# Kernel tuning notes

Hardware: AMD Instinct MI355X
Metric: run time of the kernel (lower is better)

The kernel has to match this reference:

```python
import jax, jax.numpy as jnp
import numpy as np

# Dimensions
B = 2          # batch
WIN = 8
S = WIN * WIN  # 64 tokens in the window
C = 64         # embed_dim (per-head channel dim)
NH = 8         # num_heads
H, W = 32, 32  # per-token spatial field
M1, M2 = 16, 16  # retained Fourier modes


def _spectral_conv(x, w):
    """FNO-style spectral conv over the last two dims.
    x: [B, S, Cin, H, W] real; w: [Cin, Cout, M1, M2, 2] (real/imag parts).
    rfft2 -> truncate to (M1, M2) modes -> complex channel mixing -> irfft2.
    """
    wc = w[..., 0] + 1j * w[..., 1]                      # [Cin, Cout, M1, M2]
    xf = jnp.fft.rfft2(x)                                # [B, S, Cin, H, W//2+1]
    of = jnp.einsum('bsixy,ioxy->bsoxy', xf[..., :M1, :M2], wc)
    out_f = jnp.zeros(xf.shape[:2] + (wc.shape[1], H, W // 2 + 1), dtype=of.dtype)
    out_f = out_f.at[..., :M1, :M2].set(of)
    return jnp.fft.irfft2(out_f, s=(H, W))               # [B, S, Cout, H, W]


def _log_cpb(w1, b1, w2, b2):
    """Swin-v2 style log-spaced continuous position bias.
    MLP(2 -> C -> NH) on log-spaced relative coords of the WIN x WIN window.
    Returns [NH, S, S].
    """
    g = jnp.arange(WIN)
    coords = jnp.stack(jnp.meshgrid(g, g, indexing='ij'), 0).reshape(2, -1)   # [2, S]
    rel = (coords[:, :, None] - coords[:, None, :]).astype(jnp.float32)       # [2, S, S]
    rel = jnp.transpose(rel, (1, 2, 0)) * (8.0 / (WIN - 1))                   # [S, S, 2]
    rel = jnp.sign(rel) * jnp.log2(jnp.abs(rel) + 1.0) / np.float32(np.log2(8.0))
    h = jax.nn.relu(rel @ w1 + b1)                                            # [S, S, C]
    bias = h @ w2 + b2                                                        # [S, S, NH]
    return 16.0 * jax.nn.sigmoid(jnp.transpose(bias, (2, 0, 1)))              # [NH, S, S]


def setup_inputs() -> dict:
    key = jax.random.key(0)
    k = jax.random.split(key, 8)
    def rn(kk, shape, s):
        return jax.random.normal(kk, shape, jnp.float32) * np.float32(s)
    return {
        'seq': jax.random.normal(k[0], (B, S, C, H, W), jnp.float32),
        'wq': rn(k[1], (C, C * NH, M1, M2, 2), 1.0 / C),
        'wk': rn(k[2], (C, C * NH, M1, M2, 2), 1.0 / C),
        'wv': rn(k[3], (C, C * NH, M1, M2, 2), 1.0 / C),
        'wo': rn(k[4], (C * NH, C, M1, M2, 2), 1.0 / (C * NH)),
        'cpb_w1': rn(k[5], (2, C), 0.1),
        'cpb_b1': jnp.zeros((C,), jnp.float32),
        'cpb_w2': rn(k[6], (C, NH), 0.1),
        'cpb_b2': jnp.zeros((NH,), jnp.float32),
    }


def reference(seq, wq, wk, wv, wo, cpb_w1, cpb_b1, cpb_w2, cpb_b2):
    # Spectral QKV projections: C -> NH*C channels
    q = _spectral_conv(seq, wq)   # [B, S, NH*C, H, W]
    kk = _spectral_conv(seq, wk)
    v = _spectral_conv(seq, wv)

    def unfl(f):  # [B, S, NH*C, H, W] -> [B, NH, S, C, H, W]
        return jnp.transpose(f.reshape(B, S, NH, C, H, W), (0, 2, 1, 3, 4, 5))

    q, kk, v = unfl(q), unfl(kk), unfl(v)

    bias = _log_cpb(cpb_w1, cpb_b1, cpb_w2, cpb_b2)      # [NH, S, S]
    scale = np.float32(1.0 / np.sqrt(C * H * W))
    scores = jnp.einsum('bhsdxy,bhtdxy->bhst', q, kk) * scale + bias
    attn = jax.nn.softmax(scores, axis=-1)               # [B, NH, S, S]
    o = jnp.einsum('bhst,bhtdxy->bhsdxy', attn, v)       # [B, NH, S, C, H, W]

    o = jnp.transpose(o, (0, 2, 1, 3, 4, 5)).reshape(B, S, NH * C, H, W)
    return _spectral_conv(o, wo)                         # [B, S, C, H, W]
```

## Files before the change

kernel.cpp:

```cpp
#include <hip/hip_runtime.h>
#include <math.h>


#define PI_F 3.14159265358979323846f

typedef _Float16 f16;
typedef f16 f16x8 __attribute__((ext_vector_type(8)));
typedef f16 f16x4 __attribute__((ext_vector_type(4)));
typedef float f32x4 __attribute__((ext_vector_type(4)));

#define MFMA(a, b, c) __builtin_amdgcn_mfma_f32_16x16x32_f16(a, b, c, 0, 0, 0)

__device__ __forceinline__ int swz128(int row, int slot) {
  return (row << 7) + (((slot) ^ (row & 7)) << 4);
}
__device__ __forceinline__ int swzel(int row, int col) {
  return (row << 7) + ((((col) >> 3) ^ (row & 7)) << 4) + (((col) & 7) << 1);
}

__global__ __launch_bounds__(256) void k_dft(const float* __restrict__ seq,
                                             f16* __restrict__ Xr,
                                             f16* __restrict__ Xi) {
  __shared__ float fld[32][33];
  __shared__ float2 tb[32][17];
  __shared__ float2 tw[32];
  int f = blockIdx.x;
  int tid = threadIdx.x;
  if (tid < 32) {
    float a = (2.0f * PI_F / 32.0f) * (float)tid;
    tw[tid] = make_float2(cosf(a), sinf(a));
  }
  const float4* s4 = (const float4*)(seq + (size_t)f * 1024);
  float4 v = s4[tid];
  int x0 = tid >> 3, y0 = (tid & 7) * 4;
  fld[x0][y0 + 0] = v.x; fld[x0][y0 + 1] = v.y;
  fld[x0][y0 + 2] = v.z; fld[x0][y0 + 3] = v.w;
  __syncthreads();
  for (int o = tid; o < 512; o += 256) {
    int x = o >> 4, q = o & 15;
    float re = 0.f, im = 0.f;
#pragma unroll
    for (int y = 0; y < 32; ++y) {
      float val = fld[x][y];
      float2 w = tw[(q * y) & 31];
      re = fmaf(val, w.x, re);
      im = fmaf(val, -w.y, im);
    }
    tb[x][q] = make_float2(re, im);
  }
  __syncthreads();
  int p = tid >> 4, q = tid & 15;
  float re = 0.f, im = 0.f;
#pragma unroll
  for (int x = 0; x < 32; ++x) {
    float2 t = tb[x][q];
    float2 w = tw[(p * x) & 31];
    re += w.x * t.x + w.y * t.y;
    im += w.x * t.y - w.y * t.x;
  }
  int b = f >> 12;
  int si = f & 4095;
  size_t o = (size_t)(b * 256 + tid) * 4096 + si;
  Xr[o] = (f16)re;
  Xi[o] = (f16)im;
}

__global__ __launch_bounds__(256) void k_repack_all(
    const float2* __restrict__ wq, const float2* __restrict__ wk,
    const float2* __restrict__ wv, const float2* __restrict__ wo,
    f16* __restrict__ Pqr, f16* __restrict__ Pqi, f16* __restrict__ Pkr,
    f16* __restrict__ Pki, f16* __restrict__ Pvr, f16* __restrict__ Pvi,
    f16* __restrict__ Por, f16* __restrict__ Poi) {
  __shared__ f16 tR[32][264];
  __shared__ f16 tI[32][264];
  int gid = blockIdx.x;
  int tsel = gid >> 10, rblk = gid & 1023;
  int m0 = (rblk & 7) << 5;
  int pc = rblk >> 3;
  const float2* in;
  f16 *oR, *oI;
  if (tsel == 0) { in = wq; oR = Pqr; oI = Pqi; }
  else if (tsel == 1) { in = wk; oR = Pkr; oI = Pki; }
  else if (tsel == 2) { in = wv; oR = Pvr; oI = Pvi; }
  else { in = wo; oR = Por; oI = Poi; }
  int tid = threadIdx.x;
  const float4* in4 = (const float4*)in;
#pragma unroll
  for (int it = 0; it < 16; ++it) {
    int k = it * 256 + tid;
    int fq = k & 15, rr = k >> 4;
    int row;
    if (tsel == 3) row = (((pc & 1) * 256 + rr) * 64) + (pc >> 1);
    else row = (rr & 63) * 512 + pc * 4 + (rr >> 6);
    float4 v = in4[(size_t)row * 128 + (m0 >> 1) + fq];
    int sw = (fq & 7) << 3;
    tR[2 * fq + 0][rr ^ sw] = (f16)v.x;
    tI[2 * fq + 0][rr ^ sw] = (f16)v.y;
    tR[2 * fq + 1][rr ^ sw] = (f16)v.z;
    tI[2 * fq + 1][rr ^ sw] = (f16)v.w;
  }
  __syncthreads();
  bool scaled = (tsel == 0) || (tsel == 2);
#pragma unroll
  for (int it = 0; it < 8; ++it) {
    int s = it * 256 + tid;
    int pl = s >> 10, mi = (s >> 5) & 31, j = s & 31;
    int sw = ((mi >> 1) & 7) << 3;
    f16x8 v = pl ? *(const f16x8*)&tI[mi][(j * 8) ^ sw]
                 : *(const f16x8*)&tR[mi][(j * 8) ^ sw];
    int mode = m0 + mi;
    if (scaled) {
      f16 scl = (mode == 0) ? (f16)1.0f
                            : (((mode & 15) == 0) ? (f16)0.5f : (f16)2.0f);
      v = v * scl;
      if (pl && mode == 0) v = (f16x8)(f16)0.0f;
    }
    f16* dst = pl ? oI : oR;
    *(f16x8*)&dst[(size_t)mode * 32768 + pc * 256 + j * 8] = v;
  }
}

__global__ __launch_bounds__(256, 2) void k_scores_m(
    const f16* __restrict__ Xr, const f16* __restrict__ Xi,
    const f16* __restrict__ Qwr, const f16* __restrict__ Qwi,
    const f16* __restrict__ Kwr, const f16* __restrict__ Kwi,
    float* __restrict__ scores) {
  __shared__ __align__(16) unsigned char smem[65536];
  const int P_WQR = 0, P_WQI = 8192, P_WKR = 16384, P_WKI = 24576;
  const int P_QR = 32768, P_QI = 40960, P_KR = 49152, P_KI = 57344;
  int tid = threadIdx.x;
  int w = tid >> 6, lane = tid & 63, r = lane & 15, g = lane >> 4;
  int wr = w >> 1, wc = w & 1;
  int chunk = blockIdx.x, h = blockIdx.y;
  f32x4 S[2][2][2] = {};
  for (int mm = 0; mm < 4; ++mm) {
    int m = chunk * 4 + mm;
    const float4* gqr = (const float4*)Qwr + (size_t)m * 4096 + h * 512;
    const float4* gqi = (const float4*)Qwi + (size_t)m * 4096 + h * 512;
    const float4* gkr = (const float4*)Kwr + (size_t)m * 4096 + h * 512;
    const float4* gki = (const float4*)Kwi + (size_t)m * 4096 + h * 512;
#pragma unroll
    for (int it = 0; it < 2; ++it) {
      int s = tid + it * 256;
      int lo = swz128(s >> 3, s & 7);
      *(float4*)(smem + P_WQR + lo) = gqr[s];
      *(float4*)(smem + P_WQI + lo) = gqi[s];
      *(float4*)(smem + P_WKR + lo) = gkr[s];
      *(float4*)(smem + P_WKI + lo) = gki[s];
    }
    __syncthreads();
#pragma unroll
    for (int b = 0; b < 2; ++b) {
      const f16x8* xr8 = (const f16x8*)Xr + (size_t)(b * 256 + m) * 512;
      const f16x8* xi8 = (const f16x8*)Xi + (size_t)(b * 256 + m) * 512;
      f16x8 axr[2][2], axi[2][2];
#pragma unroll
      for (int rt = 0; rt < 2; ++rt)
#pragma unroll
        for (int kt = 0; kt < 2; ++kt) {
          int idx = (32 * wr + rt * 16 + r) * 8 + kt * 4 + g;
          axr[rt][kt] = xr8[idx];
          axi[rt][kt] = xi8[idx];
        }
      {
        f32x4 cr[2][2] = {}, ci[2][2] = {};
#pragma unroll
        for (int ct = 0; ct < 2; ++ct)
#pragma unroll
          for (int kt = 0; kt < 2; ++kt) {
            int lo = swz128(32 * wc + ct * 16 + r, kt * 4 + g);
            f16x8 bwr = *(const f16x8*)(smem + P_WQR + lo);
            f16x8 bwi = *(const f16x8*)(smem + P_WQI + lo);
            f16x8 bwiN = -bwi;
#pragma unroll
            for (int rt = 0; rt < 2; ++rt) {
              cr[rt][ct] = MFMA(axr[rt][kt], bwr, cr[rt][ct]);
              cr[rt][ct] = MFMA(axi[rt][kt], bwiN, cr[rt][ct]);
              ci[rt][ct] = MFMA(axr[rt][kt], bwi, ci[rt][ct]);
              ci[rt][ct] = MFMA(axi[rt][kt], bwr, ci[rt][ct]);
            }
          }
#pragma unroll
        for (int rt = 0; rt < 2; ++rt)
#pragma unroll
          for (int ct = 0; ct < 2; ++ct)
#pragma unroll
            for (int j = 0; j < 4; ++j) {
              int row = 32 * wr + rt * 16 + g * 4 + j;
              int col = 32 * wc + ct * 16 + r;
              *(f16*)(smem + P_QR + swzel(row, col)) = (f16)cr[rt][ct][j];
              *(f16*)(smem + P_QI + swzel(row, col)) = (f16)ci[rt][ct][j];
            }
      }
      {
        f32x4 cr[2][2] = {}, ci[2][2] = {};
#pragma unroll
        for (int ct = 0; ct < 2; ++ct)
#pragma unroll
          for (int kt = 0; kt < 2; ++kt) {
            int lo = swz128(32 * wc + ct * 16 + r, kt * 4 + g);
            f16x8 bwr = *(const f16x8*)(smem + P_WKR + lo);
            f16x8 bwi = *(const f16x8*)(smem + P_WKI + lo);
            f16x8 bwiN = -bwi;
#pragma unroll
            for (int rt = 0; rt < 2; ++rt) {
              cr[rt][ct] = MFMA(axr[rt][kt], bwr, cr[rt][ct]);
              cr[rt][ct] = MFMA(axi[rt][kt], bwiN, cr[rt][ct]);
              ci[rt][ct] = MFMA(axr[rt][kt], bwi, ci[rt][ct]);
              ci[rt][ct] = MFMA(axi[rt][kt], bwr, ci[rt][ct]);
            }
          }
#pragma unroll
        for (int rt = 0; rt < 2; ++rt)
#pragma unroll
          for (int ct = 0; ct < 2; ++ct)
#pragma unroll
            for (int j = 0; j < 4; ++j) {
              int row = 32 * wr + rt * 16 + g * 4 + j;
              int col = 32 * wc + ct * 16 + r;
              *(f16*)(smem + P_KR + swzel(row, col)) = (f16)cr[rt][ct][j];
              *(f16*)(smem + P_KI + swzel(row, col)) = (f16)ci[rt][ct][j];
            }
      }
      __syncthreads();
      {
        f16x8 aqr[2][2], aqi[2][2];
#pragma unroll
        for (int rt = 0; rt < 2; ++rt)
#pragma unroll
          for (int kt = 0; kt < 2; ++kt) {
            int lo = swz128(32 * wr + rt * 16 + r, kt * 4 + g);
            aqr[rt][kt] = *(const f16x8*)(smem + P_QR + lo);
            aqi[rt][kt] = *(const f16x8*)(smem + P_QI + lo);
          }
#pragma unroll
        for (int ct = 0; ct < 2; ++ct)
#pragma unroll
          for (int kt = 0; kt < 2; ++kt) {
            int lo = swz128(32 * wc + ct * 16 + r, kt * 4 + g);
            f16x8 bkr = *(const f16x8*)(smem + P_KR + lo);
            f16x8 bki = *(const f16x8*)(smem + P_KI + lo);
#pragma unroll
            for (int rt = 0; rt < 2; ++rt) {
              S[b][rt][ct] = MFMA(aqr[rt][kt], bkr, S[b][rt][ct]);
              S[b][rt][ct] = MFMA(aqi[rt][kt], bki, S[b][rt][ct]);
            }
          }
      }
      __syncthreads();
    }
  }
  const float fac = 1.0f / 262144.0f;
#pragma unroll
  for (int b = 0; b < 2; ++b) {
    float* dst = scores + ((size_t)(b * 8 + h)) * 4096;
#pragma unroll
    for (int rt = 0; rt < 2; ++rt)
#pragma unroll
      for (int ct = 0; ct < 2; ++ct)
#pragma unroll
        for (int j = 0; j < 4; ++j) {
          int s_ = 32 * wr + rt * 16 + g * 4 + j;
          int t_ = 32 * wc + ct * 16 + r;
          atomicAdd(&dst[s_ * 64 + t_], S[b][rt][ct][j] * fac);
        }
  }
}

__global__ __launch_bounds__(64) void k_softmax(const float* __restrict__ scores,
                                                const float* __restrict__ w1,
                                                const float* __restrict__ b1,
                                                const float* __restrict__ w2,
                                                const float* __restrict__ b2,
                                                f16* __restrict__ at) {
  int id = blockIdx.x;
  int s = id & 63;
  int h = (id >> 6) & 7;
  int t = threadIdx.x;
  float d0 = (float)((s >> 3) - (t >> 3)) * (8.0f / 7.0f);
  float d1 = (float)((s & 7) - (t & 7)) * (8.0f / 7.0f);
  float a0 = log2f(fabsf(d0) + 1.0f) * (1.0f / 3.0f);
  float a1 = log2f(fabsf(d1) + 1.0f) * (1.0f / 3.0f);
  float r0 = (d0 < 0.f) ? -a0 : a0;
  float r1 = (d1 < 0.f) ? -a1 : a1;
  float acc = b2[h];
  for (int c = 0; c < 64; ++c) {
    float hv = fmaf(r0, w1[c], fmaf(r1, w1[64 + c], b1[c]));
    hv = fmaxf(hv, 0.0f);
    acc = fmaf(hv, w2[c * 8 + h], acc);
  }
  float bias = 16.0f / (1.0f + expf(-acc));
  size_t base = (size_t)id * 64;
  float v = scores[base + t] + bias;
  float mx = v;
  for (int o = 32; o; o >>= 1) mx = fmaxf(mx, __shfl_xor(mx, o));
  float e = expf(v - mx);
  float sm = e;
  for (int o = 32; o; o >>= 1) sm += __shfl_xor(sm, o);
  at[base + t] = (f16)(e / sm);
}

__global__ __launch_bounds__(256, 2) void k_vpath_m(
    const f16* __restrict__ Xr, const f16* __restrict__ Xi,
    const f16* __restrict__ Vwr, const f16* __restrict__ Vwi,
    const f16* __restrict__ Owr, const f16* __restrict__ Owi,
    const f16* __restrict__ At, float2* __restrict__ Ff) {
  __shared__ __align__(16) unsigned char smem[73728];
  const int P_WVR = 0, P_WVI = 8192, P_WOR = 16384, P_WOI = 24576;
  const int P_VTR = 32768, P_VTI = 40960, P_YR = 49152, P_YI = 57344;
  const int P_AT = 65536;
  int tid = threadIdx.x;
  int w = tid >> 6, lane = tid & 63, r = lane & 15, g = lane >> 4;
  int wr = w >> 1, wc = w & 1;
  int m = blockIdx.x, b = blockIdx.y;
  const f16x8* xr8 = (const f16x8*)Xr + (size_t)(b * 256 + m) * 512;
  const f16x8* xi8 = (const f16x8*)Xi + (size_t)(b * 256 + m) * 512;
  f16x8 axr[2][2], axi[2][2], axiN[2][2];
#pragma unroll
  for (int rt = 0; rt < 2; ++rt)
#pragma unroll
    for (int kt = 0; kt < 2; ++kt) {
      int idx = (32 * wr + rt * 16 + r) * 8 + kt * 4 + g;
      axr[rt][kt] = xr8[idx];
      axi[rt][kt] = xi8[idx];
      axiN[rt][kt] = -axi[rt][kt];
    }
  f32x4 fr[2][2] = {}, fi_[2][2] = {};
  for (int h = 0; h < 8; ++h) {
    __syncthreads();
    const float4* gvr = (const float4*)Vwr + (size_t)m * 4096 + h * 512;
    const float4* gvi = (const float4*)Vwi + (size_t)m * 4096 + h * 512;
    const float4* gor = (const float4*)Owr + (size_t)m * 4096 + h * 8;
    const float4* goi = (const float4*)Owi + (size_t)m * 4096 + h * 8;
    const float4* gat = (const float4*)At + (size_t)(b * 8 + h) * 512;
#pragma unroll
    for (int it = 0; it < 2; ++it) {
      int s = tid + it * 256;
      int row = s >> 3, sl = s & 7;
      int lo = swz128(row, sl);
      *(float4*)(smem + P_WVR + lo) = gvr[s];
      *(float4*)(smem + P_WVI + lo) = gvi[s];
      *(float4*)(smem + P_WOR + lo) = gor[row * 64 + sl];
      *(float4*)(smem + P_WOI + lo) = goi[row * 64 + sl];
      *(float4*)(smem + P_AT + lo) = gat[s];
    }
    __syncthreads();
    {
      f32x4 vr[2][2] = {}, vi[2][2] = {};
#pragma unroll
      for (int ct = 0; ct < 2; ++ct)
#pragma unroll
        for (int kt = 0; kt < 2; ++kt) {
          int lo = swz128(32 * wc + ct * 16 + r, kt * 4 + g);
          f16x8 bwr = *(const f16x8*)(smem + P_WVR + lo);
          f16x8 bwi = *(const f16x8*)(smem + P_WVI + lo);
#pragma unroll
          for (int rt = 0; rt < 2; ++rt) {
            vr[rt][ct] = MFMA(axr[rt][kt], bwr, vr[rt][ct]);
            vr[rt][ct] = MFMA(axiN[rt][kt], bwi, vr[rt][ct]);
            vi[rt][ct] = MFMA(axr[rt][kt], bwi, vi[rt][ct]);
            vi[rt][ct] = MFMA(axi[rt][kt], bwr, vi[rt][ct]);
          }
        }
#pragma unroll
      for (int rt = 0; rt < 2; ++rt)
#pragma unroll
        for (int ct = 0; ct < 2; ++ct) {
          int drow = 32 * wc + ct * 16 + r;
          int t0 = 32 * wr + rt * 16 + g * 4;
          f16x4 pr, pi;
#pragma unroll
          for (int j = 0; j < 4; ++j) {
            pr[j] = (f16)vr[rt][ct][j];
            pi[j] = (f16)vi[rt][ct][j];
          }
          int lo = swzel(drow, t0);
          *(f16x4*)(smem + P_VTR + lo) = pr;
          *(f16x4*)(smem + P_VTI + lo) = pi;
        }
    }
    __syncthreads();
    {
      f16x8 aat[2][2];
#pragma unroll
      for (int rt = 0; rt < 2; ++rt)
#pragma unroll
        for (int kt = 0; kt < 2; ++kt)
          aat[rt][kt] = *(const f16x8*)(
              smem + P_AT + swz128(32 * wr + rt * 16 + r, kt * 4 + g));
      f32x4 yr[2][2] = {}, yi[2][2] = {};
#pragma unroll
      for (int ct = 0; ct < 2; ++ct)
#pragma unroll
        for (int kt = 0; kt < 2; ++kt) {
          int lo = swz128(32 * wc + ct * 16 + r, kt * 4 + g);
          f16x8 bvr = *(const f16x8*)(smem + P_VTR + lo);
          f16x8 bvi = *(const f16x8*)(smem + P_VTI + lo);
#pragma unroll
          for (int rt = 0; rt < 2; ++rt) {
            yr[rt][ct] = MFMA(aat[rt][kt], bvr, yr[rt][ct]);
            yi[rt][ct] = MFMA(aat[rt][kt], bvi, yi[rt][ct]);
          }
        }
#pragma unroll
      for (int rt = 0; rt < 2; ++rt)
#pragma unroll
        for (int ct = 0; ct < 2; ++ct)
#pragma unroll
          for (int j = 0; j < 4; ++j) {
            int row = 32 * wr + rt * 16 + g * 4 + j;
            int col = 32 * wc + ct * 16 + r;
            *(f16*)(smem + P_YR + swzel(row, col)) = (f16)yr[rt][ct][j];
            *(f16*)(smem + P_YI + swzel(row, col)) = (f16)yi[rt][ct][j];
          }
    }
    __syncthreads();
    {
      f16x8 ayr[2][2], ayi[2][2], ayiN[2][2];
#pragma unroll
      for (int rt = 0; rt < 2; ++rt)
#pragma unroll
        for (int kt = 0; kt < 2; ++kt) {
          int lo = swz128(32 * wr + rt * 16 + r, kt * 4 + g);
          ayr[rt][kt] = *(const f16x8*)(smem + P_YR + lo);
          ayi[rt][kt] = *(const f16x8*)(smem + P_YI + lo);
          ayiN[rt][kt] = -ayi[rt][kt];
        }
#pragma unroll
      for (int ct = 0; ct < 2; ++ct)
#pragma unroll
        for (int kt = 0; kt < 2; ++kt) {
          int lo = swz128(32 * wc + ct * 16 + r, kt * 4 + g);
          f16x8 bor = *(const f16x8*)(smem + P_WOR + lo);
          f16x8 boi = *(const f16x8*)(smem + P_WOI + lo);
#pragma unroll
          for (int rt = 0; rt < 2; ++rt) {
            fr[rt][ct] = MFMA(ayr[rt][kt], bor, fr[rt][ct]);
            fr[rt][ct] = MFMA(ayiN[rt][kt], boi, fr[rt][ct]);
            fi_[rt][ct] = MFMA(ayr[rt][kt], boi, fi_[rt][ct]);
            fi_[rt][ct] = MFMA(ayi[rt][kt], bor, fi_[rt][ct]);
          }
        }
    }
  }
#pragma unroll
  for (int rt = 0; rt < 2; ++rt)
#pragma unroll
    for (int ct = 0; ct < 2; ++ct)
#pragma unroll
      for (int j = 0; j < 4; ++j) {
        int s_ = 32 * wr + rt * 16 + g * 4 + j;
        int c_ = 32 * wc + ct * 16 + r;
        Ff[(((size_t)(b * 64 + s_)) * 64 + c_) * 256 + m] =
            make_float2(fr[rt][ct][j], fi_[rt][ct][j]);
      }
}

__global__ __launch_bounds__(256) void k_idft(const float2* __restrict__ Ff,
                                              float* __restrict__ out) {
  __shared__ float2 Fm[256];
  __shared__ float2 g[32][17];
  __shared__ float2 tw[32];
  int f = blockIdx.x;
  int tid = threadIdx.x;
  if (tid < 32) {
    float a = (2.0f * PI_F / 32.0f) * (float)tid;
    tw[tid] = make_float2(cosf(a), sinf(a));
  }
  Fm[tid] = Ff[(size_t)f * 256 + tid];
  __syncthreads();
  for (int o = tid; o < 512; o += 256) {
    int x = o >> 4, q = o & 15;
    float gr = 0.f, gi = 0.f;
#pragma unroll
    for (int p = 0; p < 16; ++p) {
      float2 a = Fm[p * 16 + q];
      float2 w = tw[(p * x) & 31];
      gr += a.x * w.x - a.y * w.y;
      gi += a.x * w.y + a.y * w.x;
    }
    g[x][q] = make_float2(gr, gi);
  }
  __syncthreads();
  int x = tid >> 3, j0 = (tid & 7) * 4;
  float4 r;
  float* rr = &r.x;
#pragma unroll
  for (int jj = 0; jj < 4; ++jj) {
    int j = j0 + jj;
    float acc = 0.f;
#pragma unroll
    for (int q = 0; q < 16; ++q) {
      float2 gv = g[x][q];
      float2 w = tw[(q * j) & 31];
      acc += gv.x * w.x - gv.y * w.y;
    }
    rr[jj] = acc * (1.0f / 1024.0f);
  }
  *(float4*)(out + (size_t)f * 1024 + x * 32 + j0) = r;
}

extern "C" void kernel_launch(void* const* d_in, const int* in_sizes, int n_in,
                              void* d_out, int out_size, void* d_ws,
                              size_t ws_size, hipStream_t stream) {
  const float* seq = (const float*)d_in[0];
  const float2* wq = (const float2*)d_in[1];
  const float2* wk = (const float2*)d_in[2];
  const float2* wv = (const float2*)d_in[3];
  const float2* wo = (const float2*)d_in[4];
  const float* w1 = (const float*)d_in[5];
  const float* b1 = (const float*)d_in[6];
  const float* w2 = (const float*)d_in[7];
  const float* b2 = (const float*)d_in[8];
  float* out = (float*)d_out;

  char* ws = (char*)d_ws;
  f16* Xr = (f16*)(ws + 0);
  f16* Xi = (f16*)(ws + 4194304);
  float* scores = (float*)(ws + 8388608);
  f16* At = (f16*)(ws + 8650752);
  float2* Ff = (float2*)(ws + 8781824);
  f16* Pqr = (f16*)(ws + 25559040);
  f16* Pqi = (f16*)(ws + 42336256);
  f16* Pkr = (f16*)(ws + 59113472);
  f16* Pki = (f16*)(ws + 75890688);
  f16* Pvr = (f16*)(ws + 92667904);
  f16* Pvi = (f16*)(ws + 109445120);
  f16* Por = (f16*)(ws + 126222336);
  f16* Poi = (f16*)(ws + 142999552);

  hipMemsetAsync(scores, 0, 262144, stream);
  k_dft<<<8192, 256, 0, stream>>>(seq, Xr, Xi);
  k_repack_all<<<4096, 256, 0, stream>>>(wq, wk, wv, wo, Pqr, Pqi, Pkr, Pki,
                                         Pvr, Pvi, Por, Poi);
  k_scores_m<<<dim3(64, 8), 256, 0, stream>>>(Xr, Xi, Pqr, Pqi, Pkr, Pki,
                                              scores);
  k_softmax<<<1024, 64, 0, stream>>>(scores, w1, b1, w2, b2, At);
  k_vpath_m<<<dim3(256, 2), 256, 0, stream>>>(Xr, Xi, Pvr, Pvi, Por, Poi, At,
                                              Ff);
  k_idft<<<8192, 256, 0, stream>>>(Ff, out);
}
```

Baseline: 273.4 us.

## Merge DFT/repack/scores into heterogeneous megakernels and drop shared-memory weight staging

Combines the forward DFT with the Q/K weight repack in one launch, and the V/O repack with the score computation in a second launch, so independent work can overlap inside each grid. The repack now writes a plain row-major layout, and the scores and V-path kernels read MFMA weight fragments straight from global memory instead of staging them in LDS. This cuts shared memory and removes barriers. The V-path output is written coalesced and then reordered by a new transpose kernel. The risks are uncoalesced global fragment loads, extra traffic from the transpose, and the scores blocks being scheduled after the repack blocks inside the same grid.

```diff
diff --git a/kernel.cpp b/kernel.cpp
--- a/kernel.cpp
+++ b/kernel.cpp
@@ -18,14 +18,11 @@
   return (row << 7) + ((((col) >> 3) ^ (row & 7)) << 4) + (((col) & 7) << 1);
 }
 
-__global__ __launch_bounds__(256) void k_dft(const float* __restrict__ seq,
-                                             f16* __restrict__ Xr,
-                                             f16* __restrict__ Xi) {
-  __shared__ float fld[32][33];
-  __shared__ float2 tb[32][17];
-  __shared__ float2 tw[32];
-  int f = blockIdx.x;
-  int tid = threadIdx.x;
+__device__ void dft_body(char* sm, int f, int tid, const float* __restrict__ seq,
+                         f16* __restrict__ Xr, f16* __restrict__ Xi) {
+  float(*fld)[33] = (float(*)[33])sm;
+  float2(*tb)[17] = (float2(*)[17])(sm + 4224);
+  float2* tw = (float2*)(sm + 8576);
   if (tid < 32) {
     float a = (2.0f * PI_F / 32.0f) * (float)tid;
     tw[tid] = make_float2(cosf(a), sinf(a));
@@ -65,49 +62,25 @@
   Xi[o] = (f16)im;
 }
 
-__global__ __launch_bounds__(256) void k_repack_all(
-    const float2* __restrict__ wq, const float2* __restrict__ wk,
-    const float2* __restrict__ wv, const float2* __restrict__ wo,
-    f16* __restrict__ Pqr, f16* __restrict__ Pqi, f16* __restrict__ Pkr,
-    f16* __restrict__ Pki, f16* __restrict__ Pvr, f16* __restrict__ Pvi,
-    f16* __restrict__ Por, f16* __restrict__ Poi) {
-  __shared__ f16 tR[32][264];
-  __shared__ f16 tI[32][264];
-  int gid = blockIdx.x;
-  int tsel = gid >> 10, rblk = gid & 1023;
-  int m0 = (rblk & 7) << 5;
-  int pc = rblk >> 3;
-  const float2* in;
-  f16 *oR, *oI;
-  if (tsel == 0) { in = wq; oR = Pqr; oI = Pqi; }
-  else if (tsel == 1) { in = wk; oR = Pkr; oI = Pki; }
-  else if (tsel == 2) { in = wv; oR = Pvr; oI = Pvi; }
-  else { in = wo; oR = Por; oI = Poi; }
-  int tid = threadIdx.x;
+__device__ void repack_qkv(char* sm, int tid, int r, const float2* __restrict__ in,
+                           f16* __restrict__ oR, f16* __restrict__ oI,
+                           bool scaled) {
+  f16(*tR)[72] = (f16(*)[72])sm;
+  f16(*tI)[72] = (f16(*)[72])(sm + 9216);
+  int m0 = (r & 3) * 64, bb = r >> 2;
   const float4* in4 = (const float4*)in;
-#pragma unroll
-  for (int it = 0; it < 16; ++it) {
-    int k = it * 256 + tid;
-    int fq = k & 15, rr = k >> 4;
-    int row;
-    if (tsel == 3) row = (((pc & 1) * 256 + rr) * 64) + (pc >> 1);
-    else row = (rr & 63) * 512 + pc * 4 + (rr >> 6);
-    float4 v = in4[(size_t)row * 128 + (m0 >> 1) + fq];
-    int sw = (fq & 7) << 3;
-    tR[2 * fq + 0][rr ^ sw] = (f16)v.x;
-    tI[2 * fq + 0][rr ^ sw] = (f16)v.y;
-    tR[2 * fq + 1][rr ^ sw] = (f16)v.z;
-    tI[2 * fq + 1][rr ^ sw] = (f16)v.w;
-  }
-  __syncthreads();
-  bool scaled = (tsel == 0) || (tsel == 2);
-#pragma unroll
-  for (int it = 0; it < 8; ++it) {
-    int s = it * 256 + tid;
-    int pl = s >> 10, mi = (s >> 5) & 31, j = s & 31;
-    int sw = ((mi >> 1) & 7) << 3;
-    f16x8 v = pl ? *(const f16x8*)&tI[mi][(j * 8) ^ sw]
-                 : *(const f16x8*)&tR[mi][(j * 8) ^ sw];
+  for (int k = tid; k < 2048; k += 256) {
+    int ai = k >> 5, mj = k & 31;
+    float4 v = in4[((size_t)ai * 512 + bb) * 128 + (m0 >> 1) + mj];
+    tR[2 * mj + 0][ai] = (f16)v.x;
+    tI[2 * mj + 0][ai] = (f16)v.y;
+    tR[2 * mj + 1][ai] = (f16)v.z;
+    tI[2 * mj + 1][ai] = (f16)v.w;
+  }
+  __syncthreads();
+  for (int k = tid; k < 1024; k += 256) {
+    int pl = k >> 9, s = k & 511, mi = s >> 3, a8 = (s & 7) * 8;
+    f16x8 v = pl ? *(const f16x8*)&tI[mi][a8] : *(const f16x8*)&tR[mi][a8];
     int mode = m0 + mi;
     if (scaled) {
       f16 scl = (mode == 0) ? (f16)1.0f
@@ -116,39 +89,46 @@
       if (pl && mode == 0) v = (f16x8)(f16)0.0f;
     }
     f16* dst = pl ? oI : oR;
-    *(f16x8*)&dst[(size_t)mode * 32768 + pc * 256 + j * 8] = v;
-  }
-}
-
-__global__ __launch_bounds__(256, 2) void k_scores_m(
-    const f16* __restrict__ Xr, const f16* __restrict__ Xi,
-    const f16* __restrict__ Qwr, const f16* __restrict__ Qwi,
-    const f16* __restrict__ Kwr, const f16* __restrict__ Kwi,
-    float* __restrict__ scores) {
-  __shared__ __align__(16) unsigned char smem[65536];
-  const int P_WQR = 0, P_WQI = 8192, P_WKR = 16384, P_WKI = 24576;
-  const int P_QR = 32768, P_QI = 40960, P_KR = 49152, P_KI = 57344;
-  int tid = threadIdx.x;
+    *(f16x8*)&dst[(size_t)mode * 32768 + (size_t)bb * 64 + a8] = v;
+  }
+}
+__device__ void repack_wo(char* sm, int tid, int r, const float2* __restrict__ in,
+                          f16* __restrict__ oR, f16* __restrict__ oI) {
+  f16(*tR)[72] = (f16(*)[72])sm;
+  f16(*tI)[72] = (f16(*)[72])(sm + 9216);
+  int m0 = (r & 3) * 64;
+  int a0 = ((r >> 2) & 7) * 64;
+  int bb = r >> 5;
+  const float4* in4 = (const float4*)in;
+  for (int k = tid; k < 2048; k += 256) {
+    int ai = k >> 5, mj = k & 31;
+    float4 v = in4[((size_t)(a0 + ai) * 64 + bb) * 128 + (m0 >> 1) + mj];
+    tR[2 * mj + 0][ai] = (f16)v.x;
+    tI[2 * mj + 0][ai] = (f16)v.y;
+    tR[2 * mj + 1][ai] = (f16)v.z;
+    tI[2 * mj + 1][ai] = (f16)v.w;
+  }
+  __syncthreads();
+  for (int k = tid; k < 1024; k += 256) {
+    int pl = k >> 9, s = k & 511, mi = s >> 3, a8 = (s & 7) * 8;
+    f16x8 v = pl ? *(const f16x8*)&tI[mi][a8] : *(const f16x8*)&tR[mi][a8];
+    int mode = m0 + mi;
+    f16* dst = pl ? oI : oR;
+    *(f16x8*)&dst[(size_t)mode * 32768 + (size_t)bb * 512 + a0 + a8] = v;
+  }
+}
+
+__device__ void scores_body(char* sm, int tid, int chunk, int h,
+                            const f16* __restrict__ Xr, const f16* __restrict__ Xi,
+                            const f16* __restrict__ Qwr, const f16* __restrict__ Qwi,
+                            const f16* __restrict__ Kwr, const f16* __restrict__ Kwi,
+                            float* __restrict__ scores) {
+  const int P_QR = 0, P_QI = 8192, P_KR = 16384, P_KI = 24576;
   int w = tid >> 6, lane = tid & 63, r = lane & 15, g = lane >> 4;
   int wr = w >> 1, wc = w & 1;
-  int chunk = blockIdx.x, h = blockIdx.y;
   f32x4 S[2][2][2] = {};
   for (int mm = 0; mm < 4; ++mm) {
     int m = chunk * 4 + mm;
-    const float4* gqr = (const float4*)Qwr + (size_t)m * 4096 + h * 512;
-    const float4* gqi = (const float4*)Qwi + (size_t)m * 4096 + h * 512;
-    const float4* gkr = (const float4*)Kwr + (size_t)m * 4096 + h * 512;
-    const float4* gki = (const float4*)Kwi + (size_t)m * 4096 + h * 512;
-#pragma unroll
-    for (int it = 0; it < 2; ++it) {
-      int s = tid + it * 256;
-      int lo = swz128(s >> 3, s & 7);
-      *(float4*)(smem + P_WQR + lo) = gqr[s];
-      *(float4*)(smem + P_WQI + lo) = gqi[s];
-      *(float4*)(smem + P_WKR + lo) = gkr[s];
-      *(float4*)(smem + P_WKI + lo) = gki[s];
-    }
-    __syncthreads();
 #pragma unroll
     for (int b = 0; b < 2; ++b) {
       const f16x8* xr8 = (const f16x8*)Xr + (size_t)(b * 256 + m) * 512;
@@ -168,9 +148,11 @@
         for (int ct = 0; ct < 2; ++ct)
 #pragma unroll
           for (int kt = 0; kt < 2; ++kt) {
-            int lo = swz128(32 * wc + ct * 16 + r, kt * 4 + g);
-            f16x8 bwr = *(const f16x8*)(smem + P_WQR + lo);
-            f16x8 bwi = *(const f16x8*)(smem + P_WQI + lo);
+            size_t wb = (size_t)m * 32768 +
+                        (size_t)(h * 64 + 32 * wc + ct * 16 + r) * 64 +
+                        (kt * 4 + g) * 8;
+            f16x8 bwr = *(const f16x8*)(Qwr + wb);
+            f16x8 bwi = *(const f16x8*)(Qwi + wb);
             f16x8 bwiN = -bwi;
 #pragma unroll
             for (int rt = 0; rt < 2; ++rt) {
@@ -188,8 +170,8 @@
             for (int j = 0; j < 4; ++j) {
               int row = 32 * wr + rt * 16 + g * 4 + j;
               int col = 32 * wc + ct * 16 + r;
-              *(f16*)(smem + P_QR + swzel(row, col)) = (f16)cr[rt][ct][j];
-              *(f16*)(smem + P_QI + swzel(row, col)) = (f16)ci[rt][ct][j];
+              *(f16*)(sm + P_QR + swzel(row, col)) = (f16)cr[rt][ct][j];
+              *(f16*)(sm + P_QI + swzel(row, col)) = (f16)ci[rt][ct][j];
             }
       }
       {
@@ -198,9 +180,11 @@
         for (int ct = 0; ct < 2; ++ct)
 #pragma unroll
           for (int kt = 0; kt < 2; ++kt) {
-            int lo = swz128(32 * wc + ct * 16 + r, kt * 4 + g);
-            f16x8 bwr = *(const f16x8*)(smem + P_WKR + lo);
-            f16x8 bwi = *(const f16x8*)(smem + P_WKI + lo);
+            size_t wb = (size_t)m * 32768 +
+                        (size_t)(h * 64 + 32 * wc + ct * 16 + r) * 64 +
+                        (kt * 4 + g) * 8;
+            f16x8 bwr = *(const f16x8*)(Kwr + wb);
+            f16x8 bwi = *(const f16x8*)(Kwi + wb);
             f16x8 bwiN = -bwi;
 #pragma unroll
             for (int rt = 0; rt < 2; ++rt) {
@@ -218,8 +202,8 @@
             for (int j = 0; j < 4; ++j) {
               int row = 32 * wr + rt * 16 + g * 4 + j;
               int col = 32 * wc + ct * 16 + r;
-              *(f16*)(smem + P_KR + swzel(row, col)) = (f16)cr[rt][ct][j];
-              *(f16*)(smem + P_KI + swzel(row, col)) = (f16)ci[rt][ct][j];
+              *(f16*)(sm + P_KR + swzel(row, col)) = (f16)cr[rt][ct][j];
+              *(f16*)(sm + P_KI + swzel(row, col)) = (f16)ci[rt][ct][j];
             }
       }
       __syncthreads();
@@ -230,16 +214,16 @@
 #pragma unroll
           for (int kt = 0; kt < 2; ++kt) {
             int lo = swz128(32 * wr + rt * 16 + r, kt * 4 + g);
-            aqr[rt][kt] = *(const f16x8*)(smem + P_QR + lo);
-            aqi[rt][kt] = *(const f16x8*)(smem + P_QI + lo);
+            aqr[rt][kt] = *(const f16x8*)(sm + P_QR + lo);
+            aqi[rt][kt] = *(const f16x8*)(sm + P_QI + lo);
           }
 #pragma unroll
         for (int ct = 0; ct < 2; ++ct)
 #pragma unroll
           for (int kt = 0; kt < 2; ++kt) {
             int lo = swz128(32 * wc + ct * 16 + r, kt * 4 + g);
-            f16x8 bkr = *(const f16x8*)(smem + P_KR + lo);
-            f16x8 bki = *(const f16x8*)(smem + P_KI + lo);
+            f16x8 bkr = *(const f16x8*)(sm + P_KR + lo);
+            f16x8 bki = *(const f16x8*)(sm + P_KI + lo);
 #pragma unroll
             for (int rt = 0; rt < 2; ++rt) {
               S[b][rt][ct] = MFMA(aqr[rt][kt], bkr, S[b][rt][ct]);
@@ -264,6 +248,35 @@
           int t_ = 32 * wc + ct * 16 + r;
           atomicAdd(&dst[s_ * 64 + t_], S[b][rt][ct][j] * fac);
         }
+  }
+}
+
+__global__ __launch_bounds__(256) void k_mega1(
+    const float* __restrict__ seq, f16* __restrict__ Xr, f16* __restrict__ Xi,
+    const float2* __restrict__ wq, const float2* __restrict__ wk,
+    f16* __restrict__ Pqr, f16* __restrict__ Pqi, f16* __restrict__ Pkr,
+    f16* __restrict__ Pki) {
+  __shared__ __align__(16) char sm[18432];
+  int bx = blockIdx.x, tid = threadIdx.x;
+  if (bx < 2048) repack_qkv(sm, tid, bx, wq, Pqr, Pqi, true);
+  else if (bx < 4096) repack_qkv(sm, tid, bx - 2048, wk, Pkr, Pki, false);
+  else dft_body(sm, bx - 4096, tid, seq, Xr, Xi);
+}
+
+__global__ __launch_bounds__(256, 2) void k_mega2(
+    const f16* __restrict__ Xr, const f16* __restrict__ Xi,
+    const f16* __restrict__ Qwr, const f16* __restrict__ Qwi,
+    const f16* __restrict__ Kwr, const f16* __restrict__ Kwi,
+    float* __restrict__ scores, const float2* __restrict__ wv,
+    const float2* __restrict__ wo, f16* __restrict__ Pvr, f16* __restrict__ Pvi,
+    f16* __restrict__ Por, f16* __restrict__ Poi) {
+  __shared__ __align__(16) char sm[32768];
+  int bx = blockIdx.x, tid = threadIdx.x;
+  if (bx < 2048) repack_qkv(sm, tid, bx, wv, Pvr, Pvi, true);
+  else if (bx < 4096) repack_wo(sm, tid, bx - 2048, wo, Por, Poi);
+  else {
+    int sb = bx - 4096;
+    scores_body(sm, tid, sb & 63, sb >> 6, Xr, Xi, Qwr, Qwi, Kwr, Kwi, scores);
   }
 }
 
@@ -304,18 +317,16 @@
     const f16* __restrict__ Xr, const f16* __restrict__ Xi,
     const f16* __restrict__ Vwr, const f16* __restrict__ Vwi,
     const f16* __restrict__ Owr, const f16* __restrict__ Owi,
-    const f16* __restrict__ At, float2* __restrict__ Ff) {
-  __shared__ __align__(16) unsigned char smem[73728];
-  const int P_WVR = 0, P_WVI = 8192, P_WOR = 16384, P_WOI = 24576;
-  const int P_VTR = 32768, P_VTI = 40960, P_YR = 49152, P_YI = 57344;
-  const int P_AT = 65536;
+    const f16* __restrict__ At, float2* __restrict__ Ff2) {
+  __shared__ __align__(16) char sm[32768];
+  const int P_VTR = 0, P_VTI = 8192, P_YR = 16384, P_YI = 24576;
   int tid = threadIdx.x;
   int w = tid >> 6, lane = tid & 63, r = lane & 15, g = lane >> 4;
   int wr = w >> 1, wc = w & 1;
   int m = blockIdx.x, b = blockIdx.y;
   const f16x8* xr8 = (const f16x8*)Xr + (size_t)(b * 256 + m) * 512;
   const f16x8* xi8 = (const f16x8*)Xi + (size_t)(b * 256 + m) * 512;
-  f16x8 axr[2][2], axi[2][2], axiN[2][2];
+  f16x8 axr[2][2], axi[2][2];
 #pragma unroll
   for (int rt = 0; rt < 2; ++rt)
 #pragma unroll
@@ -323,41 +334,25 @@
       int idx = (32 * wr + rt * 16 + r) * 8 + kt * 4 + g;
       axr[rt][kt] = xr8[idx];
       axi[rt][kt] = xi8[idx];
-      axiN[rt][kt] = -axi[rt][kt];
     }
   f32x4 fr[2][2] = {}, fi_[2][2] = {};
   for (int h = 0; h < 8; ++h) {
-    __syncthreads();
-    const float4* gvr = (const float4*)Vwr + (size_t)m * 4096 + h * 512;
-    const float4* gvi = (const float4*)Vwi + (size_t)m * 4096 + h * 512;
-    const float4* gor = (const float4*)Owr + (size_t)m * 4096 + h * 8;
-    const float4* goi = (const float4*)Owi + (size_t)m * 4096 + h * 8;
-    const float4* gat = (const float4*)At + (size_t)(b * 8 + h) * 512;
-#pragma unroll
-    for (int it = 0; it < 2; ++it) {
-      int s = tid + it * 256;
-      int row = s >> 3, sl = s & 7;
-      int lo = swz128(row, sl);
-      *(float4*)(smem + P_WVR + lo) = gvr[s];
-      *(float4*)(smem + P_WVI + lo) = gvi[s];
-      *(float4*)(smem + P_WOR + lo) = gor[row * 64 + sl];
-      *(float4*)(smem + P_WOI + lo) = goi[row * 64 + sl];
-      *(float4*)(smem + P_AT + lo) = gat[s];
-    }
-    __syncthreads();
     {
       f32x4 vr[2][2] = {}, vi[2][2] = {};
 #pragma unroll
       for (int ct = 0; ct < 2; ++ct)
 #pragma unroll
         for (int kt = 0; kt < 2; ++kt) {
-          int lo = swz128(32 * wc + ct * 16 + r, kt * 4 + g);
-          f16x8 bwr = *(const f16x8*)(smem + P_WVR + lo);
-          f16x8 bwi = *(const f16x8*)(smem + P_WVI + lo);
+          size_t wb = (size_t)m * 32768 +
+                      (size_t)(h * 64 + 32 * wc + ct * 16 + r) * 64 +
+                      (kt * 4 + g) * 8;
+          f16x8 bwr = *(const f16x8*)(Vwr + wb);
+          f16x8 bwi = *(const f16x8*)(Vwi + wb);
+          f16x8 bwiN = -bwi;
 #pragma unroll
           for (int rt = 0; rt < 2; ++rt) {
             vr[rt][ct] = MFMA(axr[rt][kt], bwr, vr[rt][ct]);
-            vr[rt][ct] = MFMA(axiN[rt][kt], bwi, vr[rt][ct]);
+            vr[rt][ct] = MFMA(axi[rt][kt], bwiN, vr[rt][ct]);
             vi[rt][ct] = MFMA(axr[rt][kt], bwi, vi[rt][ct]);
             vi[rt][ct] = MFMA(axi[rt][kt], bwr, vi[rt][ct]);
           }
@@ -375,8 +370,8 @@
             pi[j] = (f16)vi[rt][ct][j];
           }
           int lo = swzel(drow, t0);
-          *(f16x4*)(smem + P_VTR + lo) = pr;
-          *(f16x4*)(smem + P_VTI + lo) = pi;
+          *(f16x4*)(sm + P_VTR + lo) = pr;
+          *(f16x4*)(sm + P_VTI + lo) = pi;
         }
     }
     __syncthreads();
@@ -386,16 +381,17 @@
       for (int rt = 0; rt < 2; ++rt)
 #pragma unroll
         for (int kt = 0; kt < 2; ++kt)
-          aat[rt][kt] = *(const f16x8*)(
-              smem + P_AT + swz128(32 * wr + rt * 16 + r, kt * 4 + g));
+          aat[rt][kt] = *(const f16x8*)(At + (size_t)(b * 8 + h) * 4096 +
+                                        (size_t)(32 * wr + rt * 16 + r) * 64 +
+                                        (kt * 4 + g) * 8);
       f32x4 yr[2][2] = {}, yi[2][2] = {};
 #pragma unroll
       for (int ct = 0; ct < 2; ++ct)
 #pragma unroll
         for (int kt = 0; kt < 2; ++kt) {
           int lo = swz128(32 * wc + ct * 16 + r, kt * 4 + g);
-          f16x8 bvr = *(const f16x8*)(smem + P_VTR + lo);
-          f16x8 bvi = *(const f16x8*)(smem + P_VTI + lo);
+          f16x8 bvr = *(const f16x8*)(sm + P_VTR + lo);
+          f16x8 bvi = *(const f16x8*)(sm + P_VTI + lo);
 #pragma unroll
           for (int rt = 0; rt < 2; ++rt) {
             yr[rt][ct] = MFMA(aat[rt][kt], bvr, yr[rt][ct]);
@@ -410,39 +406,42 @@
           for (int j = 0; j < 4; ++j) {
             int row = 32 * wr + rt * 16 + g * 4 + j;
             int col = 32 * wc + ct * 16 + r;
-            *(f16*)(smem + P_YR + swzel(row, col)) = (f16)yr[rt][ct][j];
-            *(f16*)(smem + P_YI + swzel(row, col)) = (f16)yi[rt][ct][j];
+            *(f16*)(sm + P_YR + swzel(row, col)) = (f16)yr[rt][ct][j];
+            *(f16*)(sm + P_YI + swzel(row, col)) = (f16)yi[rt][ct][j];
           }
     }
     __syncthreads();
     {
-      f16x8 ayr[2][2], ayi[2][2], ayiN[2][2];
+      f16x8 ayr[2][2], ayi[2][2];
 #pragma unroll
       for (int rt = 0; rt < 2; ++rt)
 #pragma unroll
         for (int kt = 0; kt < 2; ++kt) {
           int lo = swz128(32 * wr + rt * 16 + r, kt * 4 + g);
-          ayr[rt][kt] = *(const f16x8*)(smem + P_YR + lo);
-          ayi[rt][kt] = *(const f16x8*)(smem + P_YI + lo);
-          ayiN[rt][kt] = -ayi[rt][kt];
+          ayr[rt][kt] = *(const f16x8*)(sm + P_YR + lo);
+          ayi[rt][kt] = *(const f16x8*)(sm + P_YI + lo);
         }
 #pragma unroll
       for (int ct = 0; ct < 2; ++ct)
 #pragma unroll
         for (int kt = 0; kt < 2; ++kt) {
-          int lo = swz128(32 * wc + ct * 16 + r, kt * 4 + g);
-          f16x8 bor = *(const f16x8*)(smem + P_WOR + lo);
-          f16x8 boi = *(const f16x8*)(smem + P_WOI + lo);
+          size_t ob = (size_t)m * 32768 +
+                      (size_t)(32 * wc + ct * 16 + r) * 512 + h * 64 +
+                      (kt * 4 + g) * 8;
+          f16x8 bor = *(const f16x8*)(Owr + ob);
+          f16x8 boi = *(const f16x8*)(Owi + ob);
+          f16x8 boiN = -boi;
 #pragma unroll
           for (int rt = 0; rt < 2; ++rt) {
             fr[rt][ct] = MFMA(ayr[rt][kt], bor, fr[rt][ct]);
-            fr[rt][ct] = MFMA(ayiN[rt][kt], boi, fr[rt][ct]);
+            fr[rt][ct] = MFMA(ayi[rt][kt], boiN, fr[rt][ct]);
             fi_[rt][ct] = MFMA(ayr[rt][kt], boi, fi_[rt][ct]);
             fi_[rt][ct] = MFMA(ayi[rt][kt], bor, fi_[rt][ct]);
           }
         }
     }
   }
+  float2* dst = Ff2 + (size_t)m * 8192 + (size_t)b * 4096;
 #pragma unroll
   for (int rt = 0; rt < 2; ++rt)
 #pragma unroll
@@ -451,9 +450,24 @@
       for (int j = 0; j < 4; ++j) {
         int s_ = 32 * wr + rt * 16 + g * 4 + j;
         int c_ = 32 * wc + ct * 16 + r;
-        Ff[(((size_t)(b * 64 + s_)) * 64 + c_) * 256 + m] =
-            make_float2(fr[rt][ct][j], fi_[rt][ct][j]);
+        dst[s_ * 64 + c_] = make_float2(fr[rt][ct][j], fi_[rt][ct][j]);
       }
+}
+
+__global__ __launch_bounds__(256) void k_tr(const float2* __restrict__ Ff2,
+                                            float2* __restrict__ Fft) {
+  __shared__ float2 t[64][65];
+  int m0 = blockIdx.x * 64, f0 = blockIdx.y * 64;
+  int tid = threadIdx.x;
+  for (int k = tid; k < 4096; k += 256) {
+    int mi = k >> 6, fj = k & 63;
+    t[mi][fj] = Ff2[(size_t)(m0 + mi) * 8192 + f0 + fj];
+  }
+  __syncthreads();
+  for (int k = tid; k < 4096; k += 256) {
+    int fj = k >> 6, mi = k & 63;
+    Fft[(size_t)(f0 + fj) * 256 + m0 + mi] = t[mi][fj];
+  }
 }
 
 __global__ __launch_bounds__(256) void k_idft(const float2* __restrict__ Ff,
@@ -519,7 +533,7 @@
   f16* Xi = (f16*)(ws + 4194304);
   float* scores = (float*)(ws + 8388608);
   f16* At = (f16*)(ws + 8650752);
-  float2* Ff = (float2*)(ws + 8781824);
+  float2* Ff2 = (float2*)(ws + 8781824);
   f16* Pqr = (f16*)(ws + 25559040);
   f16* Pqi = (f16*)(ws + 42336256);
   f16* Pkr = (f16*)(ws + 59113472);
@@ -528,15 +542,15 @@
   f16* Pvi = (f16*)(ws + 109445120);
   f16* Por = (f16*)(ws + 126222336);
   f16* Poi = (f16*)(ws + 142999552);
+  float2* Fft = (float2*)(ws + 25559040);
 
   hipMemsetAsync(scores, 0, 262144, stream);
-  k_dft<<<8192, 256, 0, stream>>>(seq, Xr, Xi);
-  k_repack_all<<<4096, 256, 0, stream>>>(wq, wk, wv, wo, Pqr, Pqi, Pkr, Pki,
-                                         Pvr, Pvi, Por, Poi);
-  k_scores_m<<<dim3(64, 8), 256, 0, stream>>>(Xr, Xi, Pqr, Pqi, Pkr, Pki,
-                                              scores);
+  k_mega1<<<12288, 256, 0, stream>>>(seq, Xr, Xi, wq, wk, Pqr, Pqi, Pkr, Pki);
+  k_mega2<<<4608, 256, 0, stream>>>(Xr, Xi, Pqr, Pqi, Pkr, Pki, scores, wv, wo,
+                                    Pvr, Pvi, Por, Poi);
   k_softmax<<<1024, 64, 0, stream>>>(scores, w1, b1, w2, b2, At);
   k_vpath_m<<<dim3(256, 2), 256, 0, stream>>>(Xr, Xi, Pvr, Pvi, Por, Poi, At,
-                                              Ff);
-  k_idft<<<8192, 256, 0, stream>>>(Ff, out);
-}
+                                              Ff2);
+  k_tr<<<dim3(4, 128), 256, 0, stream>>>(Ff2, Fft);
+  k_idft<<<8192, 256, 0, stream>>>(Fft, out);
+}
```

Result: slower. 305.8 us (+11.8%).
